# Kernel tuning notes

Hardware: AMD Instinct MI355X
Metric: run time of the kernel (lower is better)

The kernel has to match this reference:

```python
import jax, jax.numpy as jnp
import numpy as np

N_NODES = 50000
IN_CH, HID_CH, OUT_CH = 256, 128, 64
N_EDGES = 800000


def setup_inputs() -> dict:
    key = jax.random.key(0)
    ks = jax.random.split(key, 8)
    x = jax.random.normal(ks[0], (N_NODES, IN_CH), dtype=jnp.float32)
    edge_index = jax.random.randint(ks[1], (2, N_EDGES), 0, N_NODES, dtype=jnp.int64)
    edge_weight = jax.random.uniform(ks[2], (N_EDGES,), dtype=jnp.float32)
    # Glorot-style init for the two GCNConv linear layers (PyG uses glorot init, zero bias)
    W1 = jax.random.normal(ks[3], (IN_CH, HID_CH), dtype=jnp.float32) * (2.0 / (IN_CH + HID_CH)) ** 0.5
    b1 = jnp.zeros((HID_CH,), dtype=jnp.float32)
    W2 = jax.random.normal(ks[4], (HID_CH, OUT_CH), dtype=jnp.float32) * (2.0 / (HID_CH + OUT_CH)) ** 0.5
    b2 = jnp.zeros((OUT_CH,), dtype=jnp.float32)
    return {"x": x, "edge_index": edge_index, "edge_weight": edge_weight,
            "W1": W1, "b1": b1, "W2": W2, "b2": b2}


def _gcn_norm(edge_index, edge_weight, num_nodes):
    # PyG gcn_norm with add_self_loops=True: append self loops (weight 1.0),
    # deg[j] = sum of incoming edge weights, norm_e = deg[src]^-1/2 * w_e * deg[dst]^-1/2
    loop = jnp.arange(num_nodes, dtype=edge_index.dtype)
    row = jnp.concatenate([edge_index[0], loop])  # source nodes
    col = jnp.concatenate([edge_index[1], loop])  # destination nodes
    w = jnp.concatenate([edge_weight, jnp.ones((num_nodes,), dtype=edge_weight.dtype)])
    deg = jax.ops.segment_sum(w, col, num_segments=num_nodes)  # [N]
    deg_inv_sqrt = jnp.where(deg > 0, jax.lax.rsqrt(jnp.where(deg > 0, deg, 1.0)), 0.0)
    norm = deg_inv_sqrt[row] * w * deg_inv_sqrt[col]  # [E+N]
    return row, col, norm


def _gcn_conv(x, W, b, row, col, norm, num_nodes):
    h = x @ W                              # [N, C_out] dense linear first (as in PyG)
    msg = h[row] * norm[:, None]           # gather + per-edge scale: [E+N, C_out]
    out = jax.ops.segment_sum(msg, col, num_segments=num_nodes)  # scatter-add to dst
    return out + b


def reference(x, edge_index, edge_weight, W1, b1, W2, b2):
    num_nodes = x.shape[0]
    row, col, norm = _gcn_norm(edge_index, edge_weight, num_nodes)
    h = _gcn_conv(x, W1, b1, row, col, norm, num_nodes)
    h = jax.nn.relu(h)
    # dropout p=0.2 is identity in eval mode (training=False)
    out = _gcn_conv(h, W2, b2, row, col, norm, num_nodes)
    return out
```

## Files before the change

### kernel.cpp

```cpp
#include <hip/hip_runtime.h>
#include <hip/hip_bf16.h>
#include <math.h>

static constexpr int NNODES = 50000;
static constexpr int NEDGES = 800000;
static constexpr int NBUCK = (NNODES + 255) >> 8;
static constexpr int MAXB = 6144;
static constexpr int GEMM1_BLKS = (NNODES + 63) / 64;
static constexpr int BIN_WGS = (NEDGES + 4095) / 4096;

typedef __attribute__((ext_vector_type(8))) short bf16x8;
typedef __attribute__((ext_vector_type(4))) float f32x4;

__device__ inline short f2bf(float f) {
  union { __hip_bfloat16 h; short s; } u;
  u.h = __float2bfloat16(f);
  return u.s;
}

__device__ inline float bf2f(short s) {
  union { unsigned int u; float f; } u;
  u.u = ((unsigned int)(unsigned short)s) << 16;
  return u.f;
}

__device__ inline void i8x8_to_f32(uint2 v, float* f) {
#pragma unroll
  for (int j = 0; j < 4; ++j) f[j] = (float)(signed char)((v.x >> (8 * j)) & 0xFF);
#pragma unroll
  for (int j = 0; j < 4; ++j) f[4 + j] = (float)(signed char)((v.y >> (8 * j)) & 0xFF);
}


template <int K, int NTOT>
__device__ inline void packW_body(const float* __restrict__ W, short* __restrict__ Wpk, int t) {
  constexpr int KF = K / 32;
  constexpr int NPF = NTOT / 16;
  if (t >= KF * NPF * 64) return;
  int f = t >> 6, l = t & 63;
  int kf = f / NPF, nfb = f % NPF;
  int col = nfb * 16 + (l & 15);
  int krow = kf * 32 + (l >> 4) * 8;
  bf16x8 bv;
#pragma unroll
  for (int i = 0; i < 8; ++i) bv[i] = f2bf(W[(size_t)(krow + i) * NTOT + col]);
  ((bf16x8*)Wpk)[t] = bv;
}

__global__ void setup_kernel(const float* __restrict__ W1, short* __restrict__ Wpk1,
                             const float* __restrict__ W2, short* __restrict__ Wpk2,
                             int* __restrict__ gcur) {
  const int bid = blockIdx.x, tid = threadIdx.x;
  if (bid < 16) {
    packW_body<256, 128>(W1, Wpk1, bid * 256 + tid);
  } else if (bid < 20) {
    packW_body<128, 64>(W2, Wpk2, (bid - 16) * 256 + tid);
  } else {
    if (tid < NBUCK) gcur[tid] = tid * MAXB;
  }
}


__device__ inline void gemm1_wave(const float* __restrict__ X, const short* __restrict__ Wpk,
                                  unsigned char* __restrict__ H, float* __restrict__ sc,
                                  int n, int rowbase, int lane) {
  constexpr int KF = 8;
  constexpr int NF = 8;
  const int lrow = lane & 15;
  const int lgrp = lane >> 4;
  const int nmax = n - 1;
  int r = rowbase + lrow;
  r = r > nmax ? nmax : r;
  const bf16x8* Wf = (const bf16x8*)Wpk;
  f32x4 acc[NF] = {};
#pragma unroll
  for (int ks = 0; ks < KF; ++ks) {
    const float* xp = X + (size_t)r * 256 + ks * 32 + lgrp * 8;
    float4 x0 = *(const float4*)xp;
    float4 x1 = *(const float4*)(xp + 4);
    bf16x8 a;
    a[0] = f2bf(x0.x);
    a[1] = f2bf(x0.y);
    a[2] = f2bf(x0.z);
    a[3] = f2bf(x0.w);
    a[4] = f2bf(x1.x);
    a[5] = f2bf(x1.y);
    a[6] = f2bf(x1.z);
    a[7] = f2bf(x1.w);
#pragma unroll
    for (int nf = 0; nf < NF; ++nf) {
      bf16x8 bfr = Wf[(ks * NF + nf) * 64 + lane];
      acc[nf] = __builtin_amdgcn_mfma_f32_16x16x32_bf16(a, bfr, acc[nf], 0, 0, 0);
    }
  }
#pragma unroll
  for (int rr = 0; rr < 4; ++rr) {
    float m = 0.f;
#pragma unroll
    for (int nf = 0; nf < NF; ++nf) m = fmaxf(m, fabsf(acc[nf][rr]));
#pragma unroll
    for (int mask = 1; mask <= 8; mask <<= 1) m = fmaxf(m, __shfl_xor(m, mask));
    const int r2 = rowbase + lgrp * 4 + rr;
    const float inv = (m > 0.f) ? 127.f / m : 0.f;
    if (r2 < n) {
      if (lrow == 0) sc[r2] = m * (1.f / 127.f);
#pragma unroll
      for (int nf = 0; nf < NF; ++nf) {
        int qv = (int)rintf(acc[nf][rr] * inv);
        qv = qv > 127 ? 127 : (qv < -127 ? -127 : qv);
        H[(size_t)r2 * 128 + nf * 16 + lrow] = (unsigned char)(signed char)qv;
      }
    }
  }
}

__global__ __launch_bounds__(256) void fused1_kernel(
    const float* __restrict__ x, const short* __restrict__ Wpk1,
    unsigned char* __restrict__ h1, float* __restrict__ sc1, int n,
    const int* __restrict__ row, const int* __restrict__ col, const float* __restrict__ w,
    int* __restrict__ gcur, int2* __restrict__ binned, int e_cnt) {
  __shared__ int rcnt[NBUCK];
  __shared__ int rcur[NBUCK];
  __shared__ int gbase[NBUCK];
  const int tid = threadIdx.x;
  if ((int)blockIdx.x < GEMM1_BLKS) {
    const int rowbase = blockIdx.x * 64 + (tid >> 6) * 16;
    gemm1_wave(x, Wpk1, h1, sc1, n, rowbase, tid & 63);
    return;
  }
  const int wg = blockIdx.x - GEMM1_BLKS;
  for (int b = tid; b < NBUCK; b += 256) {
    rcnt[b] = 0;
    rcur[b] = 0;
  }
  __syncthreads();
  const int base = wg * 4096;
  int srcs[16], dsts[16];
  float ws_[16];
#pragma unroll
  for (int j = 0; j < 16; ++j) {
    int idx = base + tid + 256 * j;
    if (idx < e_cnt) {
      srcs[j] = row[idx];
      dsts[j] = col[idx];
      ws_[j] = w[idx];
      atomicAdd(&rcnt[dsts[j] >> 8], 1);
    } else {
      dsts[j] = -1;
    }
  }
  __syncthreads();
  for (int b = tid; b < NBUCK; b += 256)
    if (rcnt[b] > 0) gbase[b] = atomicAdd(&gcur[b], rcnt[b]);
  __syncthreads();
#pragma unroll
  for (int j = 0; j < 16; ++j) {
    if (dsts[j] >= 0) {
      int b = dsts[j] >> 8;
      int dl = dsts[j] & 255;
      int pos = gbase[b] + atomicAdd(&rcur[b], 1);
      binned[pos] = make_int2((dl << 16) | srcs[j], __float_as_int(ws_[j]));
    }
  }
}


__global__ __launch_bounds__(256) void bdeg_kernel(const int2* __restrict__ binned,
                                                   const int* __restrict__ gcur,
                                                   float* __restrict__ dinv,
                                                   int* __restrict__ cntg,
                                                   int* __restrict__ bbase, int n) {
  const int b = blockIdx.x, tid = threadIdx.x;
  if (b == NBUCK) {
    __shared__ int buf[256];
    int v = (tid < NBUCK) ? gcur[tid] - tid * MAXB : 0;
    buf[tid] = v;
    __syncthreads();
    for (int off = 1; off < 256; off <<= 1) {
      int t = (tid >= off) ? buf[tid - off] : 0;
      __syncthreads();
      buf[tid] += t;
      __syncthreads();
    }
    if (tid < NBUCK) bbase[tid] = buf[tid] - v;
    return;
  }
  __shared__ float degf[256];
  __shared__ int cnt[256];
  degf[tid] = 0.f;
  cnt[tid] = 0;
  __syncthreads();
  const int bcnt = gcur[b] - b * MAXB;
  const int2* bp = binned + (size_t)b * MAXB;
  for (int i = tid; i < bcnt; i += 256) {
    int2 e = bp[i];
    int dl = (e.x >> 16) & 255;
    atomicAdd(&degf[dl], __int_as_float(e.y));
    atomicAdd(&cnt[dl], 1);
  }
  __syncthreads();
  int node = b * 256 + tid;
  if (node < n) {
    dinv[node] = 1.0f / sqrtf(degf[tid] + 1.0f);
    cntg[node] = cnt[tid];
  }
}


__global__ __launch_bounds__(256) void csrfill_kernel(
    const int2* __restrict__ binned, const int* __restrict__ gcur,
    const int* __restrict__ bbase, const float* __restrict__ dinv,
    const int* __restrict__ cntg, int* __restrict__ start,
    unsigned int* __restrict__ csr, int n) {
  __shared__ float dvL[256];
  __shared__ int cur[256];
  __shared__ int buf[256];
  const int b = blockIdx.x, tid = threadIdx.x;
  const int node = b * 256 + tid;
  int c = (node < n) ? cntg[node] : 0;
  dvL[tid] = (node < n) ? dinv[node] : 0.f;
  buf[tid] = c;
  __syncthreads();
  for (int off = 1; off < 256; off <<= 1) {
    int t = (tid >= off) ? buf[tid - off] : 0;
    __syncthreads();
    buf[tid] += t;
    __syncthreads();
  }
  int localstart = buf[tid] - c;
  const int gb = bbase[b];
  if (node < n) start[node] = gb + localstart;
  cur[tid] = localstart;
  __syncthreads();
  const int bcnt = gcur[b] - b * MAXB;
  const int2* bp = binned + (size_t)b * MAXB;
  for (int i = tid; i < bcnt; i += 256) {
    int2 e = bp[i];
    int src = e.x & 0xFFFF;
    int dl = (e.x >> 16) & 255;
    float nrm = dinv[src] * __int_as_float(e.y) * dvL[dl];
    int pos = gb + atomicAdd(&cur[dl], 1);
    csr[pos] = (unsigned int)src | ((unsigned int)(unsigned short)f2bf(nrm) << 16);
  }
}


template <int K, int NTOT, bool A_BF16>
__global__ __launch_bounds__(64, 4) void mfma_gemm_kernel(const void* __restrict__ Av,
                                                          const short* __restrict__ Wpk,
                                                          unsigned char* __restrict__ H,
                                                          float* __restrict__ sc, int n) {
  constexpr int KF = K / 32;
  constexpr int NF = NTOT / 16;
  const int lane = threadIdx.x;
  const int lrow = lane & 15;
  const int lgrp = lane >> 4;
  const int rowbase = blockIdx.x * 16;
  const int nmax = n - 1;
  int r = rowbase + lrow;
  r = r > nmax ? nmax : r;
  const bf16x8* Wf = (const bf16x8*)Wpk;
  f32x4 acc[NF] = {};

#pragma unroll
  for (int ks = 0; ks < KF; ++ks) {
    bf16x8 a;
    if (A_BF16) {
      const short* X = (const short*)Av;
      a = *(const bf16x8*)(X + (size_t)r * K + ks * 32 + lgrp * 8);
    } else {
      const float* X = (const float*)Av;
      const float* xp = X + (size_t)r * K + ks * 32 + lgrp * 8;
      float4 x0 = *(const float4*)xp;
      float4 x1 = *(const float4*)(xp + 4);
      a[0] = f2bf(x0.x);
      a[1] = f2bf(x0.y);
      a[2] = f2bf(x0.z);
      a[3] = f2bf(x0.w);
      a[4] = f2bf(x1.x);
      a[5] = f2bf(x1.y);
      a[6] = f2bf(x1.z);
      a[7] = f2bf(x1.w);
    }
#pragma unroll
    for (int nf = 0; nf < NF; ++nf) {
      bf16x8 bfr = Wf[(ks * NF + nf) * 64 + lane];
      acc[nf] = __builtin_amdgcn_mfma_f32_16x16x32_bf16(a, bfr, acc[nf], 0, 0, 0);
    }
  }

#pragma unroll
  for (int rr = 0; rr < 4; ++rr) {
    float m = 0.f;
#pragma unroll
    for (int nf = 0; nf < NF; ++nf) m = fmaxf(m, fabsf(acc[nf][rr]));
#pragma unroll
    for (int mask = 1; mask <= 8; mask <<= 1) m = fmaxf(m, __shfl_xor(m, mask));
    const int r2 = rowbase + lgrp * 4 + rr;
    const float inv = (m > 0.f) ? 127.f / m : 0.f;
    if (lrow == 0) sc[r2] = m * (1.f / 127.f);
#pragma unroll
    for (int nf = 0; nf < NF; ++nf) {
      int qv = (int)rintf(acc[nf][rr] * inv);
      qv = qv > 127 ? 127 : (qv < -127 ? -127 : qv);
      H[(size_t)r2 * NTOT + nf * 16 + lrow] = (unsigned char)(signed char)qv;
    }
  }
}


template <int CH, int TPN, bool RELU, bool OUT_BF16>
__global__ __launch_bounds__(256) void gatherq_kernel(
    const unsigned char* __restrict__ h, const float* __restrict__ sc,
    const float* __restrict__ dinv, const float* __restrict__ b,
    const int* __restrict__ start, const unsigned int* __restrict__ csr,
    void* __restrict__ outp, int n, int e_cnt) {
  constexpr int NPB = 256 / TPN;
  const int tid = threadIdx.x;
  const int q = tid % TPN;
  const int g = tid / TPN;
  const int d = blockIdx.x * NPB + g;
  if (d >= n) return;
  float s = dinv[d];
  s = s * s * sc[d];
  float f[8];
  i8x8_to_f32(*(const uint2*)(h + (size_t)d * CH + q * 8), f);
  float a0[8], a1[8], a2[8], a3[8];
#pragma unroll
  for (int j = 0; j < 8; ++j) {
    a0[j] = f[j] * s + b[q * 8 + j];
    a1[j] = 0.f;
    a2[j] = 0.f;
    a3[j] = 0.f;
  }
  const int k0 = start[d];
  const int k1 = (d + 1 < n) ? start[d + 1] : e_cnt;
  int k = k0;
  for (; k + 4 <= k1; k += 4) {
    unsigned int e0 = csr[k];
    unsigned int e1 = csr[k + 1];
    unsigned int e2 = csr[k + 2];
    unsigned int e3 = csr[k + 3];
    const int s0 = e0 & 0xFFFF, s1 = e1 & 0xFFFF, s2 = e2 & 0xFFFF, s3 = e3 & 0xFFFF;
    uint2 v0 = *(const uint2*)(h + (size_t)s0 * CH + q * 8);
    uint2 v1 = *(const uint2*)(h + (size_t)s1 * CH + q * 8);
    uint2 v2 = *(const uint2*)(h + (size_t)s2 * CH + q * 8);
    uint2 v3 = *(const uint2*)(h + (size_t)s3 * CH + q * 8);
    float n0 = bf2f((short)(e0 >> 16)) * sc[s0];
    float n1 = bf2f((short)(e1 >> 16)) * sc[s1];
    float n2 = bf2f((short)(e2 >> 16)) * sc[s2];
    float n3 = bf2f((short)(e3 >> 16)) * sc[s3];
    i8x8_to_f32(v0, f);
#pragma unroll
    for (int j = 0; j < 8; ++j) a0[j] += f[j] * n0;
    i8x8_to_f32(v1, f);
#pragma unroll
    for (int j = 0; j < 8; ++j) a1[j] += f[j] * n1;
    i8x8_to_f32(v2, f);
#pragma unroll
    for (int j = 0; j < 8; ++j) a2[j] += f[j] * n2;
    i8x8_to_f32(v3, f);
#pragma unroll
    for (int j = 0; j < 8; ++j) a3[j] += f[j] * n3;
  }
  for (; k < k1; ++k) {
    unsigned int e = csr[k];
    const int s0 = e & 0xFFFF;
    float nv = bf2f((short)(e >> 16)) * sc[s0];
    i8x8_to_f32(*(const uint2*)(h + (size_t)s0 * CH + q * 8), f);
#pragma unroll
    for (int j = 0; j < 8; ++j) a0[j] += f[j] * nv;
  }
#pragma unroll
  for (int j = 0; j < 8; ++j) a0[j] += (a1[j] + a2[j]) + a3[j];
  if (RELU) {
#pragma unroll
    for (int j = 0; j < 8; ++j) a0[j] = fmaxf(a0[j], 0.f);
  }
  if (OUT_BF16) {
    bf16x8 ov;
#pragma unroll
    for (int j = 0; j < 8; ++j) ov[j] = f2bf(a0[j]);
    *(bf16x8*)((short*)outp + (size_t)d * CH + q * 8) = ov;
  } else {
    float4* op = (float4*)outp + ((size_t)d * CH + q * 8) / 4;
    op[0] = make_float4(a0[0], a0[1], a0[2], a0[3]);
    op[1] = make_float4(a0[4], a0[5], a0[6], a0[7]);
  }
}


extern "C" void kernel_launch(void* const* d_in, const int* in_sizes, int n_in,
                              void* d_out, int out_size, void* d_ws, size_t ws_size,
                              hipStream_t stream) {
  const float* x = (const float*)d_in[0];
  const int* ei = (const int*)d_in[1];
  const float* ew = (const float*)d_in[2];
  const float* W1 = (const float*)d_in[3];
  const float* b1 = (const float*)d_in[4];
  const float* W2 = (const float*)d_in[5];
  const float* b2 = (const float*)d_in[6];
  float* outp = (float*)d_out;

  const int N = NNODES, E = NEDGES;
  const int* rowp = ei;
  const int* colp = ei + E;

  char* wsb = (char*)d_ws;
  int2* binned = (int2*)wsb;        wsb += (size_t)NBUCK * MAXB * 8;
  unsigned int* csr = (unsigned int*)wsb;  wsb += (size_t)E * 4;
  short* h1r = (short*)wsb;         wsb += (size_t)N * 128 * 2;
  unsigned char* h1 = (unsigned char*)wsb; wsb += (size_t)N * 128;
  unsigned char* h2 = (unsigned char*)wsb; wsb += (size_t)N * 64;
  short* Wpk1 = (short*)wsb;        wsb += (size_t)256 * 128 * 2;
  short* Wpk2 = (short*)wsb;        wsb += (size_t)128 * 64 * 2;
  float* sc1 = (float*)wsb;         wsb += (size_t)N * 4;
  float* sc2 = (float*)wsb;         wsb += (size_t)N * 4;
  float* dinv = (float*)wsb;        wsb += (size_t)N * 4;
  int* start = (int*)wsb;           wsb += (size_t)N * 4;
  int* cntg = (int*)wsb;            wsb += (size_t)N * 4;
  int* gcur = (int*)wsb;            wsb += (size_t)NBUCK * 4;
  int* bbase = (int*)wsb;           wsb += (size_t)NBUCK * 4;

  setup_kernel<<<21, 256, 0, stream>>>(W1, Wpk1, W2, Wpk2, gcur);

  fused1_kernel<<<GEMM1_BLKS + BIN_WGS, 256, 0, stream>>>(x, Wpk1, h1, sc1, N, rowp, colp,
                                                          ew, gcur, binned, E);

  bdeg_kernel<<<NBUCK + 1, 256, 0, stream>>>(binned, gcur, dinv, cntg, bbase, N);
  csrfill_kernel<<<NBUCK, 256, 0, stream>>>(binned, gcur, bbase, dinv, cntg, start, csr, N);

  gatherq_kernel<128, 16, true, true><<<(N + 15) / 16, 256, 0, stream>>>(
      h1, sc1, dinv, b1, start, csr, h1r, N, E);

  mfma_gemm_kernel<128, 64, true><<<(N + 15) / 16, 64, 0, stream>>>(h1r, Wpk2, h2, sc2, N);
  gatherq_kernel<64, 8, false, false><<<(N + 31) / 32, 256, 0, stream>>>(
      h2, sc2, dinv, b2, start, csr, outp, N, E);
}
```

Before: 95.26 us.

## Fuse degree and CSR-fill kernels, fold source-side normalization into per-node scales

Merges the degree computation and CSR fill into one kernel that stages each bucket's edges in shared memory and computes the bucket base by reducing earlier bucket counts, removing a launch and a second global read of the binned edges. The per-edge norm no longer multiplies dinv[src]*dinv[dst]. The source factor is folded into per-node scale arrays (scd1, sc2 premultiplied by dinv), and the destination factor is applied once per node at the end of the gather. This drops a random dinv gather per edge in CSR fill. The cost is a large shared-memory buffer per block (48KB), which may limit occupancy, plus an extra scale array.

```diff
diff --git a/kernel.cpp b/kernel.cpp
--- a/kernel.cpp
+++ b/kernel.cpp
@@ -165,82 +165,62 @@
 }
 
 
-__global__ __launch_bounds__(256) void bdeg_kernel(const int2* __restrict__ binned,
-                                                   const int* __restrict__ gcur,
-                                                   float* __restrict__ dinv,
-                                                   int* __restrict__ cntg,
-                                                   int* __restrict__ bbase, int n) {
-  const int b = blockIdx.x, tid = threadIdx.x;
-  if (b == NBUCK) {
-    __shared__ int buf[256];
-    int v = (tid < NBUCK) ? gcur[tid] - tid * MAXB : 0;
-    buf[tid] = v;
-    __syncthreads();
-    for (int off = 1; off < 256; off <<= 1) {
-      int t = (tid >= off) ? buf[tid - off] : 0;
-      __syncthreads();
-      buf[tid] += t;
-      __syncthreads();
-    }
-    if (tid < NBUCK) bbase[tid] = buf[tid] - v;
-    return;
-  }
+__global__ __launch_bounds__(256) void fused2_kernel(
+    const int2* __restrict__ binned, const int* __restrict__ gcur,
+    const float* __restrict__ sc1, float* __restrict__ dinv, float* __restrict__ scd1,
+    int* __restrict__ start, unsigned int* __restrict__ csr, int n) {
+  __shared__ int2 ebuf[MAXB];
   __shared__ float degf[256];
   __shared__ int cnt[256];
+  __shared__ int cur[256];
+  __shared__ int sbuf[256];
+  const int b = blockIdx.x, tid = threadIdx.x;
+  const int bcnt = gcur[b] - b * MAXB;
+  const int2* bp = binned + (size_t)b * MAXB;
+  for (int i = tid; i < bcnt; i += 256) ebuf[i] = bp[i];
   degf[tid] = 0.f;
   cnt[tid] = 0;
   __syncthreads();
-  const int bcnt = gcur[b] - b * MAXB;
-  const int2* bp = binned + (size_t)b * MAXB;
   for (int i = tid; i < bcnt; i += 256) {
-    int2 e = bp[i];
+    int2 e = ebuf[i];
     int dl = (e.x >> 16) & 255;
     atomicAdd(&degf[dl], __int_as_float(e.y));
     atomicAdd(&cnt[dl], 1);
   }
   __syncthreads();
-  int node = b * 256 + tid;
+  sbuf[tid] = (tid < b) ? (gcur[tid] - tid * MAXB) : 0;
+  __syncthreads();
+  for (int off = 128; off > 0; off >>= 1) {
+    if (tid < off) sbuf[tid] += sbuf[tid + off];
+    __syncthreads();
+  }
+  const int gb = sbuf[0];
+  __syncthreads();
+  const int node = b * 256 + tid;
+  float dv = 1.0f / sqrtf(degf[tid] + 1.0f);
   if (node < n) {
-    dinv[node] = 1.0f / sqrtf(degf[tid] + 1.0f);
-    cntg[node] = cnt[tid];
-  }
-}
-
-
-__global__ __launch_bounds__(256) void csrfill_kernel(
-    const int2* __restrict__ binned, const int* __restrict__ gcur,
-    const int* __restrict__ bbase, const float* __restrict__ dinv,
-    const int* __restrict__ cntg, int* __restrict__ start,
-    unsigned int* __restrict__ csr, int n) {
-  __shared__ float dvL[256];
-  __shared__ int cur[256];
-  __shared__ int buf[256];
-  const int b = blockIdx.x, tid = threadIdx.x;
-  const int node = b * 256 + tid;
-  int c = (node < n) ? cntg[node] : 0;
-  dvL[tid] = (node < n) ? dinv[node] : 0.f;
-  buf[tid] = c;
+    dinv[node] = dv;
+    scd1[node] = sc1[node] * dv;
+  }
+  sbuf[tid] = cnt[tid];
   __syncthreads();
   for (int off = 1; off < 256; off <<= 1) {
-    int t = (tid >= off) ? buf[tid - off] : 0;
+    int t = (tid >= off) ? sbuf[tid - off] : 0;
     __syncthreads();
-    buf[tid] += t;
+    sbuf[tid] += t;
     __syncthreads();
   }
-  int localstart = buf[tid] - c;
-  const int gb = bbase[b];
+  int localstart = sbuf[tid] - cnt[tid];
   if (node < n) start[node] = gb + localstart;
   cur[tid] = localstart;
   __syncthreads();
-  const int bcnt = gcur[b] - b * MAXB;
-  const int2* bp = binned + (size_t)b * MAXB;
   for (int i = tid; i < bcnt; i += 256) {
-    int2 e = bp[i];
+    int2 e = ebuf[i];
     int src = e.x & 0xFFFF;
     int dl = (e.x >> 16) & 255;
-    float nrm = dinv[src] * __int_as_float(e.y) * dvL[dl];
     int pos = gb + atomicAdd(&cur[dl], 1);
-    csr[pos] = (unsigned int)src | ((unsigned int)(unsigned short)f2bf(nrm) << 16);
+    csr[pos] = (unsigned int)src |
+               ((unsigned int)(unsigned short)f2bf(__int_as_float(e.y)) << 16);
   }
 }
 
@@ -248,6 +228,7 @@
 template <int K, int NTOT, bool A_BF16>
 __global__ __launch_bounds__(64, 4) void mfma_gemm_kernel(const void* __restrict__ Av,
                                                           const short* __restrict__ Wpk,
+                                                          const float* __restrict__ dinv,
                                                           unsigned char* __restrict__ H,
                                                           float* __restrict__ sc, int n) {
   constexpr int KF = K / 32;
@@ -298,7 +279,7 @@
     for (int mask = 1; mask <= 8; mask <<= 1) m = fmaxf(m, __shfl_xor(m, mask));
     const int r2 = rowbase + lgrp * 4 + rr;
     const float inv = (m > 0.f) ? 127.f / m : 0.f;
-    if (lrow == 0) sc[r2] = m * (1.f / 127.f);
+    if (lrow == 0) sc[r2] = m * (1.f / 127.f) * dinv[r2];
 #pragma unroll
     for (int nf = 0; nf < NF; ++nf) {
       int qv = (int)rintf(acc[nf][rr] * inv);
@@ -311,7 +292,7 @@
 
 template <int CH, int TPN, bool RELU, bool OUT_BF16>
 __global__ __launch_bounds__(256) void gatherq_kernel(
-    const unsigned char* __restrict__ h, const float* __restrict__ sc,
+    const unsigned char* __restrict__ h, const float* __restrict__ scd,
     const float* __restrict__ dinv, const float* __restrict__ b,
     const int* __restrict__ start, const unsigned int* __restrict__ csr,
     void* __restrict__ outp, int n, int e_cnt) {
@@ -321,14 +302,15 @@
   const int g = tid / TPN;
   const int d = blockIdx.x * NPB + g;
   if (d >= n) return;
-  float s = dinv[d];
-  s = s * s * sc[d];
+  const float dvd = dinv[d];
+  const float sself = scd[d] * dvd;
   float f[8];
   i8x8_to_f32(*(const uint2*)(h + (size_t)d * CH + q * 8), f);
-  float a0[8], a1[8], a2[8], a3[8];
+  float sf[8], a0[8], a1[8], a2[8], a3[8];
 #pragma unroll
   for (int j = 0; j < 8; ++j) {
-    a0[j] = f[j] * s + b[q * 8 + j];
+    sf[j] = f[j] * sself + b[q * 8 + j];
+    a0[j] = 0.f;
     a1[j] = 0.f;
     a2[j] = 0.f;
     a3[j] = 0.f;
@@ -346,10 +328,10 @@
     uint2 v1 = *(const uint2*)(h + (size_t)s1 * CH + q * 8);
     uint2 v2 = *(const uint2*)(h + (size_t)s2 * CH + q * 8);
     uint2 v3 = *(const uint2*)(h + (size_t)s3 * CH + q * 8);
-    float n0 = bf2f((short)(e0 >> 16)) * sc[s0];
-    float n1 = bf2f((short)(e1 >> 16)) * sc[s1];
-    float n2 = bf2f((short)(e2 >> 16)) * sc[s2];
-    float n3 = bf2f((short)(e3 >> 16)) * sc[s3];
+    float n0 = bf2f((short)(e0 >> 16)) * scd[s0];
+    float n1 = bf2f((short)(e1 >> 16)) * scd[s1];
+    float n2 = bf2f((short)(e2 >> 16)) * scd[s2];
+    float n3 = bf2f((short)(e3 >> 16)) * scd[s3];
     i8x8_to_f32(v0, f);
 #pragma unroll
     for (int j = 0; j < 8; ++j) a0[j] += f[j] * n0;
@@ -366,26 +348,27 @@
   for (; k < k1; ++k) {
     unsigned int e = csr[k];
     const int s0 = e & 0xFFFF;
-    float nv = bf2f((short)(e >> 16)) * sc[s0];
+    float nv = bf2f((short)(e >> 16)) * scd[s0];
     i8x8_to_f32(*(const uint2*)(h + (size_t)s0 * CH + q * 8), f);
 #pragma unroll
     for (int j = 0; j < 8; ++j) a0[j] += f[j] * nv;
   }
-#pragma unroll
-  for (int j = 0; j < 8; ++j) a0[j] += (a1[j] + a2[j]) + a3[j];
+  float out[8];
+#pragma unroll
+  for (int j = 0; j < 8; ++j) out[j] = ((a0[j] + a1[j]) + (a2[j] + a3[j])) * dvd + sf[j];
   if (RELU) {
 #pragma unroll
-    for (int j = 0; j < 8; ++j) a0[j] = fmaxf(a0[j], 0.f);
+    for (int j = 0; j < 8; ++j) out[j] = fmaxf(out[j], 0.f);
   }
   if (OUT_BF16) {
     bf16x8 ov;
 #pragma unroll
-    for (int j = 0; j < 8; ++j) ov[j] = f2bf(a0[j]);
+    for (int j = 0; j < 8; ++j) ov[j] = f2bf(out[j]);
     *(bf16x8*)((short*)outp + (size_t)d * CH + q * 8) = ov;
   } else {
     float4* op = (float4*)outp + ((size_t)d * CH + q * 8) / 4;
-    op[0] = make_float4(a0[0], a0[1], a0[2], a0[3]);
-    op[1] = make_float4(a0[4], a0[5], a0[6], a0[7]);
+    op[0] = make_float4(out[0], out[1], out[2], out[3]);
+    op[1] = make_float4(out[4], out[5], out[6], out[7]);
   }
 }
 
@@ -415,25 +398,24 @@
   short* Wpk1 = (short*)wsb;        wsb += (size_t)256 * 128 * 2;
   short* Wpk2 = (short*)wsb;        wsb += (size_t)128 * 64 * 2;
   float* sc1 = (float*)wsb;         wsb += (size_t)N * 4;
+  float* scd1 = (float*)wsb;        wsb += (size_t)N * 4;
   float* sc2 = (float*)wsb;         wsb += (size_t)N * 4;
   float* dinv = (float*)wsb;        wsb += (size_t)N * 4;
   int* start = (int*)wsb;           wsb += (size_t)N * 4;
-  int* cntg = (int*)wsb;            wsb += (size_t)N * 4;
   int* gcur = (int*)wsb;            wsb += (size_t)NBUCK * 4;
-  int* bbase = (int*)wsb;           wsb += (size_t)NBUCK * 4;
 
   setup_kernel<<<21, 256, 0, stream>>>(W1, Wpk1, W2, Wpk2, gcur);
 
   fused1_kernel<<<GEMM1_BLKS + BIN_WGS, 256, 0, stream>>>(x, Wpk1, h1, sc1, N, rowp, colp,
                                                           ew, gcur, binned, E);
 
-  bdeg_kernel<<<NBUCK + 1, 256, 0, stream>>>(binned, gcur, dinv, cntg, bbase, N);
-  csrfill_kernel<<<NBUCK, 256, 0, stream>>>(binned, gcur, bbase, dinv, cntg, start, csr, N);
+  fused2_kernel<<<NBUCK, 256, 0, stream>>>(binned, gcur, sc1, dinv, scd1, start, csr, N);
 
   gatherq_kernel<128, 16, true, true><<<(N + 15) / 16, 256, 0, stream>>>(
-      h1, sc1, dinv, b1, start, csr, h1r, N, E);
-
-  mfma_gemm_kernel<128, 64, true><<<(N + 15) / 16, 64, 0, stream>>>(h1r, Wpk2, h2, sc2, N);
+      h1, scd1, dinv, b1, start, csr, h1r, N, E);
+
+  mfma_gemm_kernel<128, 64, true><<<(N + 15) / 16, 64, 0, stream>>>(h1r, Wpk2, dinv, h2,
+                                                                    sc2, N);
   gatherq_kernel<64, 8, false, false><<<(N + 31) / 32, 256, 0, stream>>>(
       h2, sc2, dinv, b2, start, csr, outp, N, E);
 }
```

After: 101.3 us. 6.4% more time.

## Fuse layer-1 gather with layer-2 MFMA GEMM via shared memory

Applied to the files above, without the earlier changes.

Merges the layer-1 neighbor aggregation (with bias and ReLU) and the second linear layer's MFMA GEMM plus int8 quantization into one kernel. The aggregated bf16 rows for 16 nodes are staged in padded LDS and consumed directly by four waves, each computing 16 output columns, with a cross-wave row max reduction for the quantization scale. This removes the bf16 h1r round trip through global memory and one kernel launch. The cost is an extra block barrier and LDS use. The grid assumes N is divisible by 16, with no bounds guard on d.

```diff
diff --git a/kernel.cpp b/kernel.cpp
--- a/kernel.cpp
+++ b/kernel.cpp
@@ -8,6 +8,7 @@
 static constexpr int MAXB = 6144;
 static constexpr int GEMM1_BLKS = (NNODES + 63) / 64;
 static constexpr int BIN_WGS = (NEDGES + 4095) / 4096;
+static constexpr int HSTR = 136;
 
 typedef __attribute__((ext_vector_type(8))) short bf16x8;
 typedef __attribute__((ext_vector_type(4))) float f32x4;
@@ -245,65 +246,118 @@
 }
 
 
-template <int K, int NTOT, bool A_BF16>
-__global__ __launch_bounds__(64, 4) void mfma_gemm_kernel(const void* __restrict__ Av,
-                                                          const short* __restrict__ Wpk,
-                                                          unsigned char* __restrict__ H,
-                                                          float* __restrict__ sc, int n) {
-  constexpr int KF = K / 32;
-  constexpr int NF = NTOT / 16;
-  const int lane = threadIdx.x;
-  const int lrow = lane & 15;
-  const int lgrp = lane >> 4;
+__global__ __launch_bounds__(256) void glayer1_kernel(
+    const unsigned char* __restrict__ h, const float* __restrict__ sc,
+    const float* __restrict__ dinv, const float* __restrict__ b,
+    const int* __restrict__ start, const unsigned int* __restrict__ csr,
+    const short* __restrict__ Wpk2, unsigned char* __restrict__ h2,
+    float* __restrict__ sc2, int n, int e_cnt) {
+  __shared__ short hbuf[16 * HSTR];
+  __shared__ float rmax[16][4];
+  const int tid = threadIdx.x;
+  const int q = tid & 15;
+  const int g = tid >> 4;
   const int rowbase = blockIdx.x * 16;
-  const int nmax = n - 1;
-  int r = rowbase + lrow;
-  r = r > nmax ? nmax : r;
-  const bf16x8* Wf = (const bf16x8*)Wpk;
-  f32x4 acc[NF] = {};
-
-#pragma unroll
-  for (int ks = 0; ks < KF; ++ks) {
-    bf16x8 a;
-    if (A_BF16) {
-      const short* X = (const short*)Av;
-      a = *(const bf16x8*)(X + (size_t)r * K + ks * 32 + lgrp * 8);
-    } else {
-      const float* X = (const float*)Av;
-      const float* xp = X + (size_t)r * K + ks * 32 + lgrp * 8;
-      float4 x0 = *(const float4*)xp;
-      float4 x1 = *(const float4*)(xp + 4);
-      a[0] = f2bf(x0.x);
-      a[1] = f2bf(x0.y);
-      a[2] = f2bf(x0.z);
-      a[3] = f2bf(x0.w);
-      a[4] = f2bf(x1.x);
-      a[5] = f2bf(x1.y);
-      a[6] = f2bf(x1.z);
-      a[7] = f2bf(x1.w);
-    }
-#pragma unroll
-    for (int nf = 0; nf < NF; ++nf) {
-      bf16x8 bfr = Wf[(ks * NF + nf) * 64 + lane];
-      acc[nf] = __builtin_amdgcn_mfma_f32_16x16x32_bf16(a, bfr, acc[nf], 0, 0, 0);
-    }
-  }
-
-#pragma unroll
-  for (int rr = 0; rr < 4; ++rr) {
-    float m = 0.f;
-#pragma unroll
-    for (int nf = 0; nf < NF; ++nf) m = fmaxf(m, fabsf(acc[nf][rr]));
-#pragma unroll
-    for (int mask = 1; mask <= 8; mask <<= 1) m = fmaxf(m, __shfl_xor(m, mask));
-    const int r2 = rowbase + lgrp * 4 + rr;
-    const float inv = (m > 0.f) ? 127.f / m : 0.f;
-    if (lrow == 0) sc[r2] = m * (1.f / 127.f);
-#pragma unroll
-    for (int nf = 0; nf < NF; ++nf) {
-      int qv = (int)rintf(acc[nf][rr] * inv);
+  const int d = rowbase + g;
+
+  {
+    float s = dinv[d];
+    s = s * s * sc[d];
+    float f[8];
+    i8x8_to_f32(*(const uint2*)(h + (size_t)d * 128 + q * 8), f);
+    float a0[8], a1[8], a2[8], a3[8];
+#pragma unroll
+    for (int j = 0; j < 8; ++j) {
+      a0[j] = f[j] * s + b[q * 8 + j];
+      a1[j] = 0.f;
+      a2[j] = 0.f;
+      a3[j] = 0.f;
+    }
+    const int k0 = start[d];
+    const int k1 = (d + 1 < n) ? start[d + 1] : e_cnt;
+    int k = k0;
+    for (; k + 4 <= k1; k += 4) {
+      unsigned int e0 = csr[k];
+      unsigned int e1 = csr[k + 1];
+      unsigned int e2 = csr[k + 2];
+      unsigned int e3 = csr[k + 3];
+      const int s0 = e0 & 0xFFFF, s1 = e1 & 0xFFFF, s2 = e2 & 0xFFFF, s3 = e3 & 0xFFFF;
+      uint2 v0 = *(const uint2*)(h + (size_t)s0 * 128 + q * 8);
+      uint2 v1 = *(const uint2*)(h + (size_t)s1 * 128 + q * 8);
+      uint2 v2 = *(const uint2*)(h + (size_t)s2 * 128 + q * 8);
+      uint2 v3 = *(const uint2*)(h + (size_t)s3 * 128 + q * 8);
+      float n0 = bf2f((short)(e0 >> 16)) * sc[s0];
+      float n1 = bf2f((short)(e1 >> 16)) * sc[s1];
+      float n2 = bf2f((short)(e2 >> 16)) * sc[s2];
+      float n3 = bf2f((short)(e3 >> 16)) * sc[s3];
+      i8x8_to_f32(v0, f);
+#pragma unroll
+      for (int j = 0; j < 8; ++j) a0[j] += f[j] * n0;
+      i8x8_to_f32(v1, f);
+#pragma unroll
+      for (int j = 0; j < 8; ++j) a1[j] += f[j] * n1;
+      i8x8_to_f32(v2, f);
+#pragma unroll
+      for (int j = 0; j < 8; ++j) a2[j] += f[j] * n2;
+      i8x8_to_f32(v3, f);
+#pragma unroll
+      for (int j = 0; j < 8; ++j) a3[j] += f[j] * n3;
+    }
+    for (; k < k1; ++k) {
+      unsigned int e = csr[k];
+      const int s0 = e & 0xFFFF;
+      float nv = bf2f((short)(e >> 16)) * sc[s0];
+      i8x8_to_f32(*(const uint2*)(h + (size_t)s0 * 128 + q * 8), f);
+#pragma unroll
+      for (int j = 0; j < 8; ++j) a0[j] += f[j] * nv;
+    }
+    bf16x8 ov;
+#pragma unroll
+    for (int j = 0; j < 8; ++j) {
+      float v = (a0[j] + a1[j]) + (a2[j] + a3[j]);
+      ov[j] = f2bf(fmaxf(v, 0.f));
+    }
+    *(bf16x8*)&hbuf[g * HSTR + q * 8] = ov;
+  }
+  __syncthreads();
+
+  {
+    const int lane = tid & 63;
+    const int wave = tid >> 6;
+    const int lrow = lane & 15;
+    const int lgrp = lane >> 4;
+    const bf16x8* Wf = (const bf16x8*)Wpk2;
+    f32x4 acc = {};
+#pragma unroll
+    for (int ks = 0; ks < 4; ++ks) {
+      bf16x8 a = *(const bf16x8*)&hbuf[lrow * HSTR + ks * 32 + lgrp * 8];
+      bf16x8 bfr = Wf[(ks * 4 + wave) * 64 + lane];
+      acc = __builtin_amdgcn_mfma_f32_16x16x32_bf16(a, bfr, acc, 0, 0, 0);
+    }
+    float rm[4];
+#pragma unroll
+    for (int rr = 0; rr < 4; ++rr) {
+      float m = fabsf(acc[rr]);
+#pragma unroll
+      for (int mask = 1; mask <= 8; mask <<= 1) m = fmaxf(m, __shfl_xor(m, mask));
+      rm[rr] = m;
+    }
+    if (lrow == 0) {
+#pragma unroll
+      for (int rr = 0; rr < 4; ++rr) rmax[lgrp * 4 + rr][wave] = rm[rr];
+    }
+    __syncthreads();
+#pragma unroll
+    for (int rr = 0; rr < 4; ++rr) {
+      const int rowl = lgrp * 4 + rr;
+      const int r2 = rowbase + rowl;
+      float m = fmaxf(fmaxf(rmax[rowl][0], rmax[rowl][1]),
+                      fmaxf(rmax[rowl][2], rmax[rowl][3]));
+      const float inv = (m > 0.f) ? 127.f / m : 0.f;
+      if (wave == 0 && lrow == 0) sc2[r2] = m * (1.f / 127.f);
+      int qv = (int)rintf(acc[rr] * inv);
       qv = qv > 127 ? 127 : (qv < -127 ? -127 : qv);
-      H[(size_t)r2 * NTOT + nf * 16 + lrow] = (unsigned char)(signed char)qv;
+      h2[(size_t)r2 * 64 + wave * 16 + lrow] = (unsigned char)(signed char)qv;
     }
   }
 }
@@ -409,7 +463,6 @@
   char* wsb = (char*)d_ws;
   int2* binned = (int2*)wsb;        wsb += (size_t)NBUCK * MAXB * 8;
   unsigned int* csr = (unsigned int*)wsb;  wsb += (size_t)E * 4;
-  short* h1r = (short*)wsb;         wsb += (size_t)N * 128 * 2;
   unsigned char* h1 = (unsigned char*)wsb; wsb += (size_t)N * 128;
   unsigned char* h2 = (unsigned char*)wsb; wsb += (size_t)N * 64;
   short* Wpk1 = (short*)wsb;        wsb += (size_t)256 * 128 * 2;
@@ -430,10 +483,9 @@
   bdeg_kernel<<<NBUCK + 1, 256, 0, stream>>>(binned, gcur, dinv, cntg, bbase, N);
   csrfill_kernel<<<NBUCK, 256, 0, stream>>>(binned, gcur, bbase, dinv, cntg, start, csr, N);
 
-  gatherq_kernel<128, 16, true, true><<<(N + 15) / 16, 256, 0, stream>>>(
-      h1, sc1, dinv, b1, start, csr, h1r, N, E);
-
-  mfma_gemm_kernel<128, 64, true><<<(N + 15) / 16, 64, 0, stream>>>(h1r, Wpk2, h2, sc2, N);
+  glayer1_kernel<<<N / 16, 256, 0, stream>>>(h1, sc1, dinv, b1, start, csr, Wpk2, h2, sc2,
+                                             N, E);
+
   gatherq_kernel<64, 8, false, false><<<(N + 31) / 32, 256, 0, stream>>>(
       h2, sc2, dinv, b2, start, csr, outp, N, E);
 }
```

Result: faster. 92.41 us (-3.0%).
